# Performance work log

Hardware: AMD Instinct MI355X
Metric: run time of the kernel (lower is better)

## Reference

```python
import jax, jax.numpy as jnp
import numpy as np

BATCH, T, H, S, P, NH = 4, 2048, 1024, 64, 64, 8
HD = H // NH

def setup_inputs() -> dict:
    key = jax.random.key(0)
    ks = jax.random.split(key, 16)
    sH = 1.0 / np.sqrt(H)
    d = {}
    d["builder_state"] = jax.random.normal(ks[0], (BATCH, T, H), jnp.float32)
    d["base_state"] = jax.random.normal(ks[1], (BATCH, T, H), jnp.float32)
    d["input_ids"] = jax.random.randint(ks[2], (BATCH, T), 0, 32000)
    d["program_probs"] = jax.random.uniform(ks[3], (BATCH, T, P), jnp.float32)
    # SSM params (scaled from raw randn for numerical stability of the 2048-step recurrence)
    d["A"] = jax.random.normal(ks[4], (S, S), jnp.float32) * (0.5 / np.sqrt(S))
    d["Bmat"] = jax.random.normal(ks[5], (H, S), jnp.float32) * sH
    d["Cmat"] = jax.random.normal(ks[6], (S, H), jnp.float32) * (1.0 / np.sqrt(S))
    d["W_in"] = jax.random.normal(ks[7], (H, H), jnp.float32) * sH
    d["b_in"] = jnp.zeros((H,), jnp.float32)
    d["W_qkv"] = jax.random.normal(ks[8], (3 * H, H), jnp.float32) * sH
    d["b_qkv"] = jnp.zeros((3 * H,), jnp.float32)
    d["W_o"] = jax.random.normal(ks[9], (H, H), jnp.float32) * sH
    d["b_o"] = jnp.zeros((H,), jnp.float32)
    d["W_prog"] = jax.random.normal(ks[10], (H, P), jnp.float32) * (1.0 / np.sqrt(P))
    d["b_prog"] = jnp.zeros((H,), jnp.float32)
    d["g1"] = jnp.ones((H,), jnp.float32); d["beta1"] = jnp.zeros((H,), jnp.float32)
    d["g2"] = jnp.ones((H,), jnp.float32); d["beta2"] = jnp.zeros((H,), jnp.float32)
    return d

def _layernorm(x, g, b):
    mu = jnp.mean(x, axis=-1, keepdims=True)
    var = jnp.mean((x - mu) ** 2, axis=-1, keepdims=True)
    return (x - mu) * jax.lax.rsqrt(var + 1e-5) * g + b

def _mha(q_in, kv_in, W_qkv, b_qkv, W_o, b_o):
    Wq, Wk, Wv = jnp.split(W_qkv, 3, axis=0)
    bq, bk, bv = jnp.split(b_qkv, 3, axis=0)
    def heads(x, W, b):  # [B,T,H] -> [B,NH,T,HD]
        y = x @ W.T + b
        return y.reshape(y.shape[0], y.shape[1], NH, HD).transpose(0, 2, 1, 3)
    q, k, v = heads(q_in, Wq, bq), heads(kv_in, Wk, bk), heads(kv_in, Wv, bv)
    scores = jnp.einsum('bhqd,bhkd->bhqk', q, k) * (1.0 / np.sqrt(HD))
    attn = jax.nn.softmax(scores, axis=-1)
    out = jnp.einsum('bhqk,bhkd->bhqd', attn, v)
    out = out.transpose(0, 2, 1, 3).reshape(q_in.shape)
    return out @ W_o.T + b_o

def reference(builder_state, base_state, input_ids, program_probs,
              A, Bmat, Cmat, W_in, b_in, W_qkv, b_qkv, W_o, b_o,
              W_prog, b_prog, g1, beta1, g2, beta2):
    # cross-attention sublayer (norm1 shared between builder and base states)
    residual = builder_state
    x = _layernorm(builder_state, g1, beta1)
    base_n = _layernorm(base_state, g1, beta1)
    x = residual + _mha(x, base_n, W_qkv, b_qkv, W_o, b_o)
    # SSM sublayer: state_{t} = silu(A @ state_{t-1}) + B^T u_t ; y_t = state_t @ C
    residual = x
    xn = _layernorm(x, g2, beta2)
    U = (xn @ W_in.T + b_in) @ Bmat            # [B,T,S] precomputed input drive
    def step(s, u_t):                           # s: [B,S], u_t: [B,S]
        s = jax.nn.silu(s @ A.T) + u_t
        return s, s
    _, states = jax.lax.scan(step, jnp.zeros((builder_state.shape[0], S), U.dtype),
                             U.transpose(1, 0, 2))  # states: [T,B,S]
    ssm_out = jnp.einsum('tbs,sh->bth', states, Cmat)
    x = residual + ssm_out
    # program modulation
    mod = program_probs.mean(axis=1) @ W_prog.T + b_prog   # [B,H]
    return x + mod[:, None, :]
```

## Files before the change

### kernel.cpp

```cpp
#include <hip/hip_runtime.h>
#include <cstdint>
#include <cstddef>

typedef unsigned short u16;
typedef short bf16x8 __attribute__((ext_vector_type(8)));
typedef float f32x4 __attribute__((ext_vector_type(4)));
typedef u16 u16x4 __attribute__((ext_vector_type(4)));
typedef u16 u16x8 __attribute__((ext_vector_type(8)));

#define DEVFN static __device__ __forceinline__

DEVFN u16 f32_to_bf16(float f){
  unsigned u = __float_as_uint(f);
  u += 0x7fffu + ((u >> 16) & 1u);
  return (u16)(u >> 16);
}

DEVFN f32x4 mfma16(bf16x8 a, bf16x8 b, f32x4 c){
  return __builtin_amdgcn_mfma_f32_16x16x32_bf16(a, b, c, 0, 0, 0);
}

__global__ void cast4_kernel(const float4* __restrict__ src, u16x4* __restrict__ dst, int n4){
  for (int i = blockIdx.x*blockDim.x + threadIdx.x; i < n4; i += gridDim.x*blockDim.x){
    float4 v = src[i];
    u16x4 o; o[0]=f32_to_bf16(v.x); o[1]=f32_to_bf16(v.y); o[2]=f32_to_bf16(v.z); o[3]=f32_to_bf16(v.w);
    dst[i] = o;
  }
}

__global__ void tcast_kernel(const float* __restrict__ Cm, u16* __restrict__ CmT){
  int i = blockIdx.x*256 + threadIdx.x;
  int h = i >> 6, s = i & 63;
  CmT[i] = f32_to_bf16(Cm[s*1024 + h]);
}

__global__ __launch_bounds__(256,1) void wcomb_kernel(const float* __restrict__ W_in,
    const float* __restrict__ Bm, u16* __restrict__ WcT){
  const int kl = threadIdx.x & 63, sl = threadIdx.x >> 6;
  const int k = ((blockIdx.x & 15) << 6) + kl;
  const int s = ((blockIdx.x >> 4) << 2) + sl;
  float a = 0.f;
#pragma unroll 8
  for (int jj = 0; jj < 1024; jj++) a = fmaf(W_in[jj*1024 + k], Bm[jj*64 + s], a);
  WcT[s*1024 + k] = f32_to_bf16(a);
}

__global__ void ubias_kernel(const float* __restrict__ b_in, const float* __restrict__ Bm,
                             float* __restrict__ ub){
  const int s = threadIdx.x;
  float a = 0.f;
  for (int jj = 0; jj < 1024; jj++) a = fmaf(b_in[jj], Bm[jj*64 + s], a);
  ub[s] = a;
}

__global__ __launch_bounds__(256,1) void ln_bf16_kernel(
    const float* __restrict__ src, u16* __restrict__ dst,
    const float* __restrict__ g, const float* __restrict__ beta)
{
  const int row = blockIdx.x, t = threadIdx.x;
  const float4 v = ((const float4*)(src + (size_t)row*1024))[t];
  float s1 = v.x+v.y+v.z+v.w;
  float s2 = v.x*v.x+v.y*v.y+v.z*v.z+v.w*v.w;
#pragma unroll
  for (int off = 32; off > 0; off >>= 1){ s1 += __shfl_xor(s1, off); s2 += __shfl_xor(s2, off); }
  __shared__ float w1[4], w2[4];
  if ((t & 63) == 0){ w1[t>>6] = s1; w2[t>>6] = s2; }
  __syncthreads();
  s1 = (w1[0]+w1[1])+(w1[2]+w1[3]);
  s2 = (w2[0]+w2[1])+(w2[2]+w2[3]);
  const float mean = s1*(1.f/1024.f);
  const float var  = s2*(1.f/1024.f) - mean*mean;
  const float rstd = rsqrtf(var + 1e-5f);
  const float4 gv = ((const float4*)g)[t];
  const float4 bv = ((const float4*)beta)[t];
  u16x4 o;
  o[0] = f32_to_bf16((v.x-mean)*rstd*gv.x + bv.x);
  o[1] = f32_to_bf16((v.y-mean)*rstd*gv.y + bv.y);
  o[2] = f32_to_bf16((v.z-mean)*rstd*gv.z + bv.z);
  o[3] = f32_to_bf16((v.w-mean)*rstd*gv.w + bv.w);
  *(u16x4*)&dst[(size_t)row*1024 + t*4] = o;
}

template<int BM,int BN,int WM,int WN,int MT,int NT,int EPI>
__global__ __launch_bounds__(256,1) void gemm_bt(
    const u16* __restrict__ Ag, const u16* __restrict__ Bg,
    void* __restrict__ Cout, const float* __restrict__ bias,
    const float* __restrict__ resid, const float* __restrict__ modv,
    int M, int N, int K)
{
  static_assert(BM == WM*MT*16 && BN == WN*NT*16 && WM*WN == 4, "tile config");
  __shared__ u16 As[BM*40];
  __shared__ u16 Bs[BN*40];
  const int t = threadIdx.x;
  const int lane = t & 63, wave = t >> 6;
  const int wm = wave / WN, wn = wave % WN;
  const int lrow = lane & 15, lq = lane >> 4;
  const int m0 = blockIdx.y * BM, n0 = blockIdx.x * BN;

  f32x4 acc[MT][NT];
#pragma unroll
  for (int i = 0; i < MT; i++)
#pragma unroll
    for (int j = 0; j < NT; j++){ acc[i][j][0]=0.f; acc[i][j][1]=0.f; acc[i][j][2]=0.f; acc[i][j][3]=0.f; }

  for (int kt = 0; kt < K; kt += 32){
#pragma unroll
    for (int i = 0; i < BM/64; i++){
      int idx = t + i*256;
      int r = idx >> 2, c = (idx & 3) << 3;
      *(u16x8*)&As[r*40 + c] = *(const u16x8*)&Ag[(size_t)(m0 + r)*K + kt + c];
    }
#pragma unroll
    for (int i = 0; i < BN/64; i++){
      int idx = t + i*256;
      int r = idx >> 2, c = (idx & 3) << 3;
      *(u16x8*)&Bs[r*40 + c] = *(const u16x8*)&Bg[(size_t)(n0 + r)*K + kt + c];
    }
    __syncthreads();
    bf16x8 af[MT], bfr[NT];
#pragma unroll
    for (int mt = 0; mt < MT; mt++)
      af[mt] = *(const bf16x8*)&As[(wm*MT*16 + mt*16 + lrow)*40 + lq*8];
#pragma unroll
    for (int nt = 0; nt < NT; nt++)
      bfr[nt] = *(const bf16x8*)&Bs[(wn*NT*16 + nt*16 + lrow)*40 + lq*8];
#pragma unroll
    for (int mt = 0; mt < MT; mt++)
#pragma unroll
      for (int nt = 0; nt < NT; nt++)
        acc[mt][nt] = mfma16(af[mt], bfr[nt], acc[mt][nt]);
    __syncthreads();
  }
  const int rb = m0 + wm*MT*16;
  const int cb = n0 + wn*NT*16;
#pragma unroll
  for (int mt = 0; mt < MT; mt++){
#pragma unroll
    for (int nt = 0; nt < NT; nt++){
#pragma unroll
      for (int r = 0; r < 4; r++){
        int row = rb + mt*16 + lq*4 + r;
        int col = cb + nt*16 + lrow;
        float v = acc[mt][nt][r];
        if (EPI & 2) v += bias[col];
        if (EPI & 4) v += resid[(size_t)row*N + col];
        if (EPI & 8) v += modv[(row >> 11)*1024 + col];
        if (EPI & 1) ((u16*)Cout)[(size_t)row*N + col] = f32_to_bf16(v);
        else         ((float*)Cout)[(size_t)row*N + col] = v;
      }
    }
  }
}

__global__ __launch_bounds__(256,1) void flash_attn(
    const u16* __restrict__ Qb, const u16* __restrict__ KVb, u16* __restrict__ Ob)
{
  __shared__ u16 Ks[64*128];
  __shared__ unsigned Vt2[128*34];
  __shared__ u16 Ps[4][16*68];
  const int t = threadIdx.x;
  const int lane = t & 63, wave = t >> 6;
  const int lrow = lane & 15, lq = lane >> 4;
  const int b = blockIdx.y >> 3, h = blockIdx.y & 7;
  const int q0 = blockIdx.x * 64;
  const float C1 = 0.08838834764831845f * 1.4426950408889634f;

  bf16x8 qf[4];
  {
    int grow = b*2048 + q0 + wave*16 + lrow;
#pragma unroll
    for (int ks = 0; ks < 4; ks++)
      qf[ks] = *(const bf16x8*)&Qb[(size_t)grow*1024 + h*128 + ks*32 + lq*8];
  }
  float lsum[4] = {0.f,0.f,0.f,0.f};
  f32x4 Oa[8];
#pragma unroll
  for (int i = 0; i < 8; i++){ Oa[i][0]=0.f; Oa[i][1]=0.f; Oa[i][2]=0.f; Oa[i][3]=0.f; }

  const int key_k = t >> 2, cg = t & 3;
  const int kp = t & 31, dg = t >> 5;

  const size_t KSTEP = (size_t)64*2048;
  const u16* Kpg = &KVb[(size_t)(b*2048 + key_k)*2048 + h*128];
  const u16* Vpg = &KVb[(size_t)(b*2048 + kp*2)*2048 + h*128 + 1024 + dg*16];

  u16x8 kreg[4];
  u16x8 vreg[4];

#pragma unroll
  for (int i = 0; i < 4; i++) kreg[i] = *(const u16x8*)&Kpg[(cg*4+i)*8];
  vreg[0] = *(const u16x8*)&Vpg[0];
  vreg[1] = *(const u16x8*)&Vpg[8];
  vreg[2] = *(const u16x8*)&Vpg[2048];
  vreg[3] = *(const u16x8*)&Vpg[2048+8];
#pragma unroll
  for (int i = 0; i < 4; i++){
    int ch = cg*4 + i;
    int ph = ch ^ (key_k & 7);
    *(u16x8*)&Ks[key_k*128 + ph*8] = kreg[i];
  }
#pragma unroll
  for (int jj = 0; jj < 8; jj++){
    Vt2[(dg*16+jj)*34 + kp]   = (unsigned)vreg[0][jj] | ((unsigned)vreg[2][jj] << 16);
    Vt2[(dg*16+8+jj)*34 + kp] = (unsigned)vreg[1][jj] | ((unsigned)vreg[3][jj] << 16);
  }

  for (int kt = 0; kt < 32; kt++){
    __syncthreads();
    if (kt < 31){
      const u16* kpg = Kpg + (size_t)(kt+1)*KSTEP;
#pragma unroll
      for (int i = 0; i < 4; i++) kreg[i] = *(const u16x8*)&kpg[(cg*4+i)*8];
      const u16* vg = Vpg + (size_t)(kt+1)*KSTEP;
      vreg[0] = *(const u16x8*)&vg[0];
      vreg[1] = *(const u16x8*)&vg[8];
      vreg[2] = *(const u16x8*)&vg[2048];
      vreg[3] = *(const u16x8*)&vg[2048+8];
    }

    f32x4 sacc[4];
    __builtin_amdgcn_s_setprio(1);
#pragma unroll
    for (int nt = 0; nt < 4; nt++){
      f32x4 a; a[0]=0.f; a[1]=0.f; a[2]=0.f; a[3]=0.f;
#pragma unroll
      for (int ks = 0; ks < 4; ks++){
        int ph = (ks*4 + lq) ^ (lrow & 7);
        bf16x8 kf = *(const bf16x8*)&Ks[(nt*16+lrow)*128 + ph*8];
        a = mfma16(qf[ks], kf, a);
      }
      sacc[nt] = a;
    }
    __builtin_amdgcn_s_setprio(0);
#pragma unroll
    for (int nt = 0; nt < 4; nt++)
#pragma unroll
      for (int r = 0; r < 4; r++){
        float p = exp2f(sacc[nt][r]*C1);
        lsum[r] += p;
        Ps[wave][(lq*4+r)*68 + nt*16 + lrow] = f32_to_bf16(p);
      }
    __builtin_amdgcn_s_setprio(1);
#pragma unroll
    for (int ks2 = 0; ks2 < 2; ks2++){
      bf16x8 pa;
      ((u16x4*)&pa)[0] = *(const u16x4*)&Ps[wave][lrow*68 + ks2*32 + lq*8];
      ((u16x4*)&pa)[1] = *(const u16x4*)&Ps[wave][lrow*68 + ks2*32 + lq*8 + 4];
#pragma unroll
      for (int nt2 = 0; nt2 < 8; nt2++){
        bf16x8 vf;
        int dwoff = (nt2*16+lrow)*34 + ks2*16 + lq*4;
        ((uint2*)&vf)[0] = *(const uint2*)&Vt2[dwoff];
        ((uint2*)&vf)[1] = *(const uint2*)&Vt2[dwoff+2];
        Oa[nt2] = mfma16(pa, vf, Oa[nt2]);
      }
    }
    __builtin_amdgcn_s_setprio(0);
    __syncthreads();
    if (kt < 31){
#pragma unroll
      for (int i = 0; i < 4; i++){
        int ch = cg*4 + i;
        int ph = ch ^ (key_k & 7);
        *(u16x8*)&Ks[key_k*128 + ph*8] = kreg[i];
      }
#pragma unroll
      for (int jj = 0; jj < 8; jj++){
        Vt2[(dg*16+jj)*34 + kp]   = (unsigned)vreg[0][jj] | ((unsigned)vreg[2][jj] << 16);
        Vt2[(dg*16+8+jj)*34 + kp] = (unsigned)vreg[1][jj] | ((unsigned)vreg[3][jj] << 16);
      }
    }
  }
#pragma unroll
  for (int r = 0; r < 4; r++){
#pragma unroll
    for (int off = 1; off < 16; off <<= 1) lsum[r] += __shfl_xor(lsum[r], off);
  }
  float inv[4];
#pragma unroll
  for (int r = 0; r < 4; r++) inv[r] = 1.0f / lsum[r];
  const int growb = b*2048 + q0 + wave*16;
#pragma unroll
  for (int nt2 = 0; nt2 < 8; nt2++)
#pragma unroll
    for (int r = 0; r < 4; r++){
      float o = Oa[nt2][r]*inv[r];
      Ob[(size_t)(growb + lq*4 + r)*1024 + h*128 + nt2*16 + lrow] = f32_to_bf16(o);
    }
}

__global__ __launch_bounds__(64,1) void scan_chunk_kernel(
    const float* __restrict__ U, const float* __restrict__ A, u16* __restrict__ S)
{
  const int b = blockIdx.y, c = blockIdx.x, j = threadIdx.x;
  float Ar[64];
#pragma unroll
  for (int k = 0; k < 64; k++) Ar[k] = A[j*64 + k];
  const float* Ub = U + (size_t)b*2048*64;
  u16* Sb = S + (size_t)b*2048*64;
  const int tout = c*32;
  const int tend = tout + 32;
  int t0 = tout - 48; if (t0 < 0) t0 = 0;
  __shared__ float sbuf[2][64];
  sbuf[0][j] = 0.f;
  __syncthreads();
  float unext = Ub[t0*64 + j];
  const float NLOG2E = -1.4426950408889634f;
  for (int t = t0; t < tend; t++){
    const int cur = (t - t0) & 1;
    f32x4 sv[16];
#pragma unroll
    for (int r = 0; r < 16; r++) sv[r] = *((const f32x4*)&sbuf[cur][r*4]);
    float u = unext;
    int tn = t + 1; if (tn >= tend) tn = tend - 1;
    unext = Ub[tn*64 + j];
    float a0=0.f, a1=0.f, a2=0.f, a3=0.f;
#pragma unroll
    for (int r = 0; r < 16; r++){
      a0 = fmaf(Ar[4*r+0], sv[r][0], a0);
      a1 = fmaf(Ar[4*r+1], sv[r][1], a1);
      a2 = fmaf(Ar[4*r+2], sv[r][2], a2);
      a3 = fmaf(Ar[4*r+3], sv[r][3], a3);
    }
    float y = (a0+a1)+(a2+a3);
    float e = exp2f(y*NLOG2E);
    float s = fmaf(y, __builtin_amdgcn_rcpf(1.f + e), u);
    sbuf[cur^1][j] = s;
    if (t >= tout) Sb[t*64 + j] = f32_to_bf16(s);
  }
}

__global__ __launch_bounds__(256,1) void pmean1_kernel(const float* __restrict__ pp,
                                                       float* __restrict__ partial){
  const int c = blockIdx.x, b = blockIdx.y, t = threadIdx.x;
  const int p = t & 63, g = t >> 6;
  const float* basep = pp + (size_t)b*2048*64 + (size_t)c*64*64;
  float s = 0.f;
#pragma unroll
  for (int i = g*16; i < g*16 + 16; i++) s += basep[i*64 + p];
  __shared__ float red[256];
  red[t] = s;
  __syncthreads();
  if (t < 64) partial[(b*32 + c)*64 + t] = (red[t] + red[64+t]) + (red[128+t] + red[192+t]);
}

__global__ void pmean2_kernel(const float* __restrict__ partial, float* __restrict__ pm){
  const int b = blockIdx.x, p = threadIdx.x;
  float s = 0.f;
#pragma unroll
  for (int c = 0; c < 32; c++) s += partial[(b*32 + c)*64 + p];
  pm[b*64 + p] = s * (1.f/2048.f);
}

__global__ void mod_kernel(const float* __restrict__ pm, const float* __restrict__ Wp,
                           const float* __restrict__ bp, float* __restrict__ mo){
  const int i = blockIdx.x*256 + threadIdx.x;
  const int b = i >> 10, hc = i & 1023;
  float s = bp[hc];
#pragma unroll 8
  for (int p = 0; p < 64; p++) s = fmaf(pm[b*64+p], Wp[hc*64+p], s);
  mo[i] = s;
}

extern "C" void kernel_launch(void* const* d_in, const int* in_sizes, int n_in,
                              void* d_out, int out_size, void* d_ws, size_t ws_size,
                              hipStream_t stream)
{
  (void)in_sizes; (void)n_in; (void)out_size; (void)ws_size;
  const float* builder = (const float*)d_in[0];
  const float* base    = (const float*)d_in[1];
  const float* pp      = (const float*)d_in[3];
  const float* Amat    = (const float*)d_in[4];
  const float* Bmat    = (const float*)d_in[5];
  const float* Cmat    = (const float*)d_in[6];
  const float* W_in    = (const float*)d_in[7];
  const float* b_in    = (const float*)d_in[8];
  const float* W_qkv   = (const float*)d_in[9];
  const float* b_qkv   = (const float*)d_in[10];
  const float* W_o     = (const float*)d_in[11];
  const float* b_o     = (const float*)d_in[12];
  const float* W_prog  = (const float*)d_in[13];
  const float* b_prog  = (const float*)d_in[14];
  const float* g1      = (const float*)d_in[15];
  const float* beta1   = (const float*)d_in[16];
  const float* g2      = (const float*)d_in[17];
  const float* beta2   = (const float*)d_in[18];
  float* out = (float*)d_out;

  char* ws = (char*)d_ws;
  const size_t MB = (size_t)1 << 20;
  u16*   Qb   = (u16*)  (ws + 0*MB);
  u16*   KVb  = (u16*)  (ws + 16*MB);
  float* Xf   = (float*)(ws + 48*MB);
  u16*   QN   = (u16*)  (ws + 80*MB);
  u16*   KVN  = (u16*)  (ws + 96*MB);
  u16*   Wq16 = (u16*)  (ws + 112*MB);
  u16*   Wo16 = (u16*)  (ws + 118*MB);
  u16*   WcT  = (u16*)  (ws + 120*MB);
  u16*   CmT  = (u16*)  (ws + 120*MB + 256*1024);
  float* Uf   = (float*)(ws + 121*MB);
  u16*   Sb   = (u16*)  (ws + 123*MB);
  float* ub   = (float*)(ws + 124*MB);
  float* pmv  = (float*)(ws + 124*MB + 4096);
  float* modv = (float*)(ws + 124*MB + 8192);
  float* ppart= (float*)(ws + 124*MB + 32768);

  cast4_kernel<<<1024,256,0,stream>>>((const float4*)W_qkv, (u16x4*)Wq16, 3145728/4);
  cast4_kernel<<<1024,256,0,stream>>>((const float4*)W_o,   (u16x4*)Wo16, 1048576/4);
  tcast_kernel<<<256,256,0,stream>>>(Cmat, CmT);
  wcomb_kernel<<<256,256,0,stream>>>(W_in, Bmat, WcT);
  ubias_kernel<<<1,64,0,stream>>>(b_in, Bmat, ub);

  ln_bf16_kernel<<<8192,256,0,stream>>>(builder, QN,  g1, beta1);
  ln_bf16_kernel<<<8192,256,0,stream>>>(base,    KVN, g1, beta1);

  gemm_bt<128,128,2,2,4,4,3><<<dim3(8,64),256,0,stream>>>(QN,  Wq16,              Qb,  b_qkv,      nullptr, nullptr, 8192,1024,1024);
  gemm_bt<128,128,2,2,4,4,3><<<dim3(16,64),256,0,stream>>>(KVN, Wq16 + 1024*1024, KVb, b_qkv+1024, nullptr, nullptr, 8192,2048,1024);

  flash_attn<<<dim3(32,32),256,0,stream>>>(Qb, KVb, QN);

  gemm_bt<128,128,2,2,4,4,6><<<dim3(8,64),256,0,stream>>>(QN, Wo16, Xf, b_o, builder, nullptr, 8192,1024,1024);

  ln_bf16_kernel<<<8192,256,0,stream>>>(Xf, KVN, g2, beta2);

  gemm_bt<64,64,2,2,2,2,2><<<dim3(1,128),256,0,stream>>>(KVN, WcT, Uf, ub, nullptr, nullptr, 8192,64,1024);

  scan_chunk_kernel<<<dim3(64,4),64,0,stream>>>(Uf, Amat, Sb);

  pmean1_kernel<<<dim3(32,4),256,0,stream>>>(pp, ppart);
  pmean2_kernel<<<4,64,0,stream>>>(ppart, pmv);
  mod_kernel<<<16,256,0,stream>>>(pmv, W_prog, b_prog, modv);

  gemm_bt<128,128,2,2,4,4,12><<<dim3(8,64),256,0,stream>>>(Sb, CmT, out, nullptr, Xf, modv, 8192,1024,64);
}
```

Measured before the change: 631.2 us.

## Keep attention probabilities in registers via transposed QK MFMA and lane shuffles

Swaps the MFMA operand order so the score tile comes out transposed, which lets each lane pack its probabilities into bf16 pairs and build the PV A-operand with cross-lane shuffles. This removes the per-wave LDS staging buffer for P. The softmax scale times log2(e) is folded into the Q projection GEMM epilogue, so the exp2 in the inner loop no longer needs a multiply. Row sums become a single scalar per lane and are redistributed at the end, at the cost of several shuffles per k-step and a Q tensor that is stored pre-scaled in bf16.

Result: slower. 644.1 us (+2.1%).

```diff
diff --git a/kernel.cpp b/kernel.cpp
--- a/kernel.cpp
+++ b/kernel.cpp
@@ -143,6 +143,7 @@
         int col = cb + nt*16 + lrow;
         float v = acc[mt][nt][r];
         if (EPI & 2) v += bias[col];
+        if (EPI & 16) v *= (0.08838834764831845f * 1.4426950408889634f);
         if (EPI & 4) v += resid[(size_t)row*N + col];
         if (EPI & 8) v += modv[(row >> 11)*1024 + col];
         if (EPI & 1) ((u16*)Cout)[(size_t)row*N + col] = f32_to_bf16(v);
@@ -157,13 +158,11 @@
 {
   __shared__ u16 Ks[64*128];
   __shared__ unsigned Vt2[128*34];
-  __shared__ u16 Ps[4][16*68];
   const int t = threadIdx.x;
   const int lane = t & 63, wave = t >> 6;
   const int lrow = lane & 15, lq = lane >> 4;
   const int b = blockIdx.y >> 3, h = blockIdx.y & 7;
   const int q0 = blockIdx.x * 64;
-  const float C1 = 0.08838834764831845f * 1.4426950408889634f;
 
   bf16x8 qf[4];
   {
@@ -172,13 +171,17 @@
     for (int ks = 0; ks < 4; ks++)
       qf[ks] = *(const bf16x8*)&Qb[(size_t)grow*1024 + h*128 + ks*32 + lq*8];
   }
-  float lsum[4] = {0.f,0.f,0.f,0.f};
+  float lsum = 0.f;
   f32x4 Oa[8];
 #pragma unroll
   for (int i = 0; i < 8; i++){ Oa[i][0]=0.f; Oa[i][1]=0.f; Oa[i][2]=0.f; Oa[i][3]=0.f; }
 
   const int key_k = t >> 2, cg = t & 3;
   const int kp = t & 31, dg = t >> 5;
+
+  const int srcA = lrow + ((lane & 16) << 1);
+  const int srcB = srcA + 16;
+  const int hi2  = lq >> 1;
 
   const size_t KSTEP = (size_t)64*2048;
   const u16* Kpg = &KVb[(size_t)(b*2048 + key_k)*2048 + h*128];
@@ -227,25 +230,40 @@
       for (int ks = 0; ks < 4; ks++){
         int ph = (ks*4 + lq) ^ (lrow & 7);
         bf16x8 kf = *(const bf16x8*)&Ks[(nt*16+lrow)*128 + ph*8];
-        a = mfma16(qf[ks], kf, a);
+        a = mfma16(kf, qf[ks], a);
       }
       sacc[nt] = a;
     }
     __builtin_amdgcn_s_setprio(0);
-#pragma unroll
-    for (int nt = 0; nt < 4; nt++)
-#pragma unroll
-      for (int r = 0; r < 4; r++){
-        float p = exp2f(sacc[nt][r]*C1);
-        lsum[r] += p;
-        Ps[wave][(lq*4+r)*68 + nt*16 + lrow] = f32_to_bf16(p);
-      }
+
+    unsigned pk[4][2];
+#pragma unroll
+    for (int nt = 0; nt < 4; nt++){
+      float p0 = exp2f(sacc[nt][0]);
+      float p1 = exp2f(sacc[nt][1]);
+      float p2 = exp2f(sacc[nt][2]);
+      float p3 = exp2f(sacc[nt][3]);
+      lsum += (p0+p1)+(p2+p3);
+      asm("v_cvt_pk_bf16_f32 %0, %1, %2" : "=v"(pk[nt][0]) : "v"(p0), "v"(p1));
+      asm("v_cvt_pk_bf16_f32 %0, %1, %2" : "=v"(pk[nt][1]) : "v"(p2), "v"(p3));
+    }
+
     __builtin_amdgcn_s_setprio(1);
 #pragma unroll
     for (int ks2 = 0; ks2 < 2; ks2++){
+      int d0a = __shfl((int)pk[2*ks2][0],   srcA);
+      int d0b = __shfl((int)pk[2*ks2+1][0], srcA);
+      int d1a = __shfl((int)pk[2*ks2][1],   srcA);
+      int d1b = __shfl((int)pk[2*ks2+1][1], srcA);
+      int d2a = __shfl((int)pk[2*ks2][0],   srcB);
+      int d2b = __shfl((int)pk[2*ks2+1][0], srcB);
+      int d3a = __shfl((int)pk[2*ks2][1],   srcB);
+      int d3b = __shfl((int)pk[2*ks2+1][1], srcB);
       bf16x8 pa;
-      ((u16x4*)&pa)[0] = *(const u16x4*)&Ps[wave][lrow*68 + ks2*32 + lq*8];
-      ((u16x4*)&pa)[1] = *(const u16x4*)&Ps[wave][lrow*68 + ks2*32 + lq*8 + 4];
+      ((int*)&pa)[0] = hi2 ? d0b : d0a;
+      ((int*)&pa)[1] = hi2 ? d1b : d1a;
+      ((int*)&pa)[2] = hi2 ? d2b : d2a;
+      ((int*)&pa)[3] = hi2 ? d3b : d3a;
 #pragma unroll
       for (int nt2 = 0; nt2 < 8; nt2++){
         bf16x8 vf;
@@ -271,14 +289,12 @@
       }
     }
   }
-#pragma unroll
-  for (int r = 0; r < 4; r++){
-#pragma unroll
-    for (int off = 1; off < 16; off <<= 1) lsum[r] += __shfl_xor(lsum[r], off);
-  }
+  lsum += __shfl_xor(lsum, 16);
+  lsum += __shfl_xor(lsum, 32);
+  float invq = 1.0f / lsum;
   float inv[4];
 #pragma unroll
-  for (int r = 0; r < 4; r++) inv[r] = 1.0f / lsum[r];
+  for (int r = 0; r < 4; r++) inv[r] = __shfl(invq, lq*4 + r);
   const int growb = b*2048 + q0 + wave*16;
 #pragma unroll
   for (int nt2 = 0; nt2 < 8; nt2++)
@@ -414,7 +430,7 @@
   ln_bf16_kernel<<<8192,256,0,stream>>>(builder, QN,  g1, beta1);
   ln_bf16_kernel<<<8192,256,0,stream>>>(base,    KVN, g1, beta1);
 
-  gemm_bt<128,128,2,2,4,4,3><<<dim3(8,64),256,0,stream>>>(QN,  Wq16,              Qb,  b_qkv,      nullptr, nullptr, 8192,1024,1024);
+  gemm_bt<128,128,2,2,4,4,19><<<dim3(8,64),256,0,stream>>>(QN,  Wq16,              Qb,  b_qkv,      nullptr, nullptr, 8192,1024,1024);
   gemm_bt<128,128,2,2,4,4,3><<<dim3(16,64),256,0,stream>>>(KVN, Wq16 + 1024*1024, KVb, b_qkv+1024, nullptr, nullptr, 8192,2048,1024);
 
   flash_attn<<<dim3(32,32),256,0,stream>>>(Qb, KVb, QN);
```
